# Kernel tuning notes

Hardware: AMD Instinct MI355X
Metric: run time of the kernel (lower is better)

Reference implementation:

```python
import jax, jax.numpy as jnp
import numpy as np

B, S, D, H = 2, 2048, 512, 8
HD = D // H
EPS = 1e-5


def _ln(x, g, b):
    mu = jnp.mean(x, axis=-1, keepdims=True)
    var = jnp.mean((x - mu) ** 2, axis=-1, keepdims=True)
    return (x - mu) * jax.lax.rsqrt(var + EPS) * g + b


def setup_inputs() -> dict:
    key = jax.random.key(0)
    ks = jax.random.split(key, 16)
    x = jax.random.normal(ks[0], (B, S, D), dtype=jnp.float32)
    adj = jax.random.randint(ks[1], (B, S, S), 0, 2, dtype=jnp.int32)
    adj = adj.at[:, jnp.arange(S), jnp.arange(S)].set(1)  # self-loops, avoid all-masked rows
    edge_attr = jax.random.normal(ks[2], (B, S, S), dtype=jnp.float32)
    sc = 1.0 / np.sqrt(D)
    p = lambda k, shp: jax.random.normal(k, shp, dtype=jnp.float32) * sc
    return {
        "x": x, "adj_matrix": adj, "edge_attr_matrix": edge_attr,
        "ln1_g": jnp.ones((D,)), "ln1_b": jnp.zeros((D,)),
        "ln2_g": jnp.ones((D,)), "ln2_b": jnp.zeros((D,)),
        "wq": p(ks[3], (D, D)), "bq": jnp.zeros((D,)),
        "wk": p(ks[4], (D, D)), "bk": jnp.zeros((D,)),
        "wv": p(ks[5], (D, D)), "bv": jnp.zeros((D,)),
        "wo": p(ks[6], (D, D)), "bo": jnp.zeros((D,)),
        "w1": p(ks[7], (D, 4 * D)), "b1": jnp.zeros((4 * D,)),
        "w2": p(ks[8], (4 * D, D)), "b2": jnp.zeros((D,)),
    }


def reference(x, adj_matrix, edge_attr_matrix, ln1_g, ln1_b, ln2_g, ln2_b,
              wq, bq, wk, bk, wv, bv, wo, bo, w1, b1, w2, b2):
    b, s, d = x.shape
    residual = x
    nx = _ln(x, ln1_g, ln1_b)
    q = (nx @ wq + bq).reshape(b, s, H, HD).transpose(0, 2, 1, 3)  # [B,H,S,HD]
    k = (nx @ wk + bk).reshape(b, s, H, HD).transpose(0, 2, 1, 3)
    v = (nx @ wv + bv).reshape(b, s, H, HD).transpose(0, 2, 1, 3)
    adjf = adj_matrix.astype(jnp.float32)
    # bias: -inf where no edge, else 0.1*edge_attr*adj (faithful to score_mod)
    bias = jnp.where(adj_matrix > 0, 0.1 * edge_attr_matrix * adjf, -jnp.inf)[:, None]  # [B,1,S,S]
    scores = jnp.einsum('bhqd,bhkd->bhqk', q, k) / np.sqrt(HD) + bias
    attn = jax.nn.softmax(scores, axis=-1)
    out = jnp.einsum('bhqk,bhkd->bhqd', attn, v)
    out = out.transpose(0, 2, 1, 3).reshape(b, s, d)
    x1 = residual + (out @ wo + bo)
    n2 = _ln(x1, ln2_g, ln2_b)
    mlp = jax.nn.gelu(n2 @ w1 + b1, approximate=False) @ w2 + b2
    return x1 + mlp
```

## Files before the change

kernel.cpp:

```cpp
#include <hip/hip_runtime.h>
#include <cstdint>
#include <cstddef>

typedef __bf16 bf16x8 __attribute__((ext_vector_type(8)));
typedef float f32x4 __attribute__((ext_vector_type(4)));
typedef const __attribute__((address_space(1))) void* gas_t;
typedef __attribute__((address_space(3))) void* las_t;

#define LOG2E 1.4426950408889634f
#define QSCALE 0.18033688011112042f
#define BSCALE 0.14426950408889634f

__device__ __forceinline__ unsigned short f2bf(float f) {
  union { float f; unsigned u; } v; v.f = f;
  unsigned r = v.u + 0x7FFFu + ((v.u >> 16) & 1u);
  return (unsigned short)(r >> 16);
}
__device__ __forceinline__ unsigned short f2bf_fast(float f) {
  union { float f; unsigned u; } v; v.f = f;
  return (unsigned short)((v.u + 0x8000u) >> 16);
}
__device__ __forceinline__ float bf2f(unsigned short h) {
  union { unsigned u; float f; } v; v.u = ((unsigned)h) << 16;
  return v.f;
}
__device__ __forceinline__ void gll16(const void* g, void* l) {
  __builtin_amdgcn_global_load_lds((gas_t)g, (las_t)l, 16, 0, 0);
}

__global__ __launch_bounds__(256) void transpose_cast(const float* __restrict__ in,
                                                      unsigned short* __restrict__ out,
                                                      int R, int C) {
  __shared__ float tile[32][33];
  int bx = blockIdx.x * 32, by = blockIdx.y * 32;
  int tx = threadIdx.x & 31, tg = threadIdx.x >> 5;
  #pragma unroll
  for (int i = 0; i < 4; i++) {
    int r = tg * 4 + i;
    tile[r][tx] = in[(size_t)(by + r) * C + bx + tx];
  }
  __syncthreads();
  #pragma unroll
  for (int i = 0; i < 4; i++) {
    int r = tg * 4 + i;
    out[(size_t)(bx + r) * R + by + tx] = f2bf(tile[tx][r]);
  }
}

struct TP4 { const float* in[4]; unsigned short* out[4]; };
__global__ __launch_bounds__(256) void transpose_cast4(TP4 p) {
  __shared__ float tile[32][33];
  const float* in = p.in[blockIdx.z];
  unsigned short* out = p.out[blockIdx.z];
  int bx = blockIdx.x * 32, by = blockIdx.y * 32;
  int tx = threadIdx.x & 31, tg = threadIdx.x >> 5;
  #pragma unroll
  for (int i = 0; i < 4; i++) {
    int r = tg * 4 + i;
    tile[r][tx] = in[(size_t)(by + r) * 512 + bx + tx];
  }
  __syncthreads();
  #pragma unroll
  for (int i = 0; i < 4; i++) {
    int r = tg * 4 + i;
    out[(size_t)(bx + r) * 512 + by + tx] = f2bf(tile[tx][r]);
  }
}

__global__ __launch_bounds__(256) void bias_pack(const int* __restrict__ adj,
                                                 const float* __restrict__ edge,
                                                 unsigned short* __restrict__ bp) {
  size_t i = ((size_t)blockIdx.x * 256 + threadIdx.x) * 4;
  int4 a = *(const int4*)(adj + i);
  float4 e = *(const float4*)(edge + i);
  ushort4 r;
  r.x = a.x > 0 ? f2bf(BSCALE * e.x * (float)a.x - 20.0f) : f2bf(-30000.0f);
  r.y = a.y > 0 ? f2bf(BSCALE * e.y * (float)a.y - 20.0f) : f2bf(-30000.0f);
  r.z = a.z > 0 ? f2bf(BSCALE * e.z * (float)a.z - 20.0f) : f2bf(-30000.0f);
  r.w = a.w > 0 ? f2bf(BSCALE * e.w * (float)a.w - 20.0f) : f2bf(-30000.0f);
  *(ushort4*)(bp + i) = r;
}

__global__ __launch_bounds__(256) void ln_kernel(const float* __restrict__ x,
                                                 const float* __restrict__ g,
                                                 const float* __restrict__ bt,
                                                 unsigned short* __restrict__ out,
                                                 const float* __restrict__ badd,
                                                 float* __restrict__ oinit) {
  int row = blockIdx.x, tid = threadIdx.x;
  const float* xr = x + (size_t)row * 512;
  float2 v = *(const float2*)(xr + tid * 2);
  float s = v.x + v.y, s2 = v.x * v.x + v.y * v.y;
  #pragma unroll
  for (int m = 1; m < 64; m <<= 1) { s += __shfl_xor(s, m, 64); s2 += __shfl_xor(s2, m, 64); }
  __shared__ float red[8];
  int w = tid >> 6;
  if ((tid & 63) == 0) { red[w * 2] = s; red[w * 2 + 1] = s2; }
  __syncthreads();
  float ts = red[0] + red[2] + red[4] + red[6];
  float ts2 = red[1] + red[3] + red[5] + red[7];
  float mu = ts * (1.0f / 512.0f);
  float rs = rsqrtf(ts2 * (1.0f / 512.0f) - mu * mu + 1e-5f);
  int c = tid * 2;
  ushort2 o;
  o.x = f2bf((v.x - mu) * rs * g[c] + bt[c]);
  o.y = f2bf((v.y - mu) * rs * g[c + 1] + bt[c + 1]);
  *(ushort2*)(out + (size_t)row * 512 + c) = o;
  if (oinit) {
    float2 oi; oi.x = v.x + badd[c]; oi.y = v.y + badd[c + 1];
    *(float2*)(oinit + (size_t)row * 512 + c) = oi;
  }
}

struct EpiQKV {
  unsigned short *q, *k, *v;
  const float *bq, *bk, *bv;
  __device__ void operator()(int m, int n, float val) const {
    int b = m >> 11, s = m & 2047;
    int which = n >> 9, col = n & 511;
    int h = col >> 6, d = col & 63;
    int bh = b * 8 + h;
    if (which == 0)      q[((size_t)bh * 2048 + s) * 64 + d] = f2bf((val + bq[col]) * QSCALE);
    else if (which == 1) k[((size_t)bh * 2048 + s) * 64 + d] = f2bf(val + bk[col]);
    else                 v[((size_t)bh * 2048 + s) * 64 + d] = f2bf(val + bv[col]);
  }
};
struct EpiAtomic {
  float* dst; int ldn;
  __device__ void operator()(int m, int n, float val) const {
    atomicAdd(dst + (size_t)m * ldn + n, val);
  }
};
struct EpiGelu {
  const float* b1; unsigned short* h;
  __device__ void operator()(int m, int n, float val) const {
    float t = val + b1[n];
    float gl = 0.5f * t * (1.0f + erff(t * 0.70710678118654752f));
    h[(size_t)m * 2048 + n] = f2bf(gl);
  }
};

template <typename Epi>
__global__ __launch_bounds__(256) void gemm_bt(const unsigned short* __restrict__ A,
                                               const unsigned short* __restrict__ Bt,
                                               int lda, int ldb, int kchunk, Epi epi) {
  __shared__ unsigned short a_lds[128 * 32];
  __shared__ unsigned short b_lds[128 * 32];
  const int tid = threadIdx.x;
  const int lane = tid & 63;
  const int w = tid >> 6;
  const int l15 = lane & 15, quad = lane >> 4;
  const int wm = w >> 1, wn = w & 1;
  const int m0 = blockIdx.y * 128, n0 = blockIdx.x * 128;
  const int K0 = blockIdx.z * kchunk, K1 = K0 + kchunk;

  f32x4 acc[4][4] = {};

  for (int k0 = K0; k0 < K1; k0 += 32) {
    __syncthreads();
    #pragma unroll
    for (int i = 0; i < 2; i++) {
      int c = tid + i * 256;
      int g = c >> 6;
      int row = g * 16 + l15;
      int col = quad * 8;
      gll16(A + (size_t)(m0 + row) * lda + k0 + col, a_lds + (size_t)(c & ~63) * 8);
      gll16(Bt + (size_t)(n0 + row) * ldb + k0 + col, b_lds + (size_t)(c & ~63) * 8);
    }
    __syncthreads();
    bf16x8 af[4], bfr[4];
    #pragma unroll
    for (int t = 0; t < 4; t++) {
      af[t]  = *(const bf16x8*)(a_lds + ((size_t)(wm * 4 + t) * 64 + lane) * 8);
      bfr[t] = *(const bf16x8*)(b_lds + ((size_t)(wn * 4 + t) * 64 + lane) * 8);
    }
    #pragma unroll
    for (int mt = 0; mt < 4; mt++)
      #pragma unroll
      for (int nt = 0; nt < 4; nt++)
        acc[mt][nt] = __builtin_amdgcn_mfma_f32_16x16x32_bf16(af[mt], bfr[nt], acc[mt][nt], 0, 0, 0);
  }
  #pragma unroll
  for (int mt = 0; mt < 4; mt++)
    #pragma unroll
    for (int nt = 0; nt < 4; nt++)
      #pragma unroll
      for (int r = 0; r < 4; r++)
        epi(m0 + wm * 64 + mt * 16 + quad * 4 + r, n0 + wn * 64 + nt * 16 + l15, acc[mt][nt][r]);
}

__global__ __launch_bounds__(256) void vt_kernel(const unsigned short* __restrict__ vb,
                                                 unsigned short* __restrict__ vbT) {
  __shared__ unsigned short tile[64][72];
  const int bh = blockIdx.y, s0 = blockIdx.x * 64;
  const int tid = threadIdx.x;
  const unsigned short* src = vb + ((size_t)bh * 2048 + s0) * 64;
  #pragma unroll
  for (int i = 0; i < 2; i++) {
    int r = (tid >> 3) + i * 32;
    int c8 = (tid & 7) * 8;
    *(uint4*)(&tile[r][c8]) = *(const uint4*)(src + (size_t)r * 64 + c8);
  }
  __syncthreads();
  unsigned short* dst = vbT + (size_t)bh * 64 * 2048 + s0;
  #pragma unroll
  for (int i = 0; i < 2; i++) {
    int d = (tid >> 3) + i * 32;
    int s8 = (tid & 7) * 8;
    ushort4 o0, o1;
    o0.x = tile[s8 + 0][d]; o0.y = tile[s8 + 1][d]; o0.z = tile[s8 + 2][d]; o0.w = tile[s8 + 3][d];
    o1.x = tile[s8 + 4][d]; o1.y = tile[s8 + 5][d]; o1.z = tile[s8 + 6][d]; o1.w = tile[s8 + 7][d];
    *(ushort4*)(dst + (size_t)d * 2048 + s8) = o0;
    *(ushort4*)(dst + (size_t)d * 2048 + s8 + 4) = o1;
  }
}

__global__ __launch_bounds__(256) void attn_kernel(const unsigned short* __restrict__ Q,
                                                   const unsigned short* __restrict__ Kb,
                                                   const unsigned short* __restrict__ VT,
                                                   const unsigned short* __restrict__ biasp,
                                                   float* __restrict__ o_part,
                                                   float* __restrict__ l_part) {
  __shared__ unsigned short k_lds[64 * 64];
  __shared__ unsigned short v_lds[64 * 64];
  __shared__ unsigned short bias_lds[128 * 72];
  __shared__ unsigned short p_lds[4][2][16 * 72];

  const int tid = threadIdx.x;
  const int lane = tid & 63, w = tid >> 6;
  const int l15 = lane & 15, quad = lane >> 4;
  const int bh = blockIdx.x, b = bh >> 3;
  const int q0 = blockIdx.y * 128;
  const int split = blockIdx.z;

  bf16x8 qf[2][2];
  #pragma unroll
  for (int g = 0; g < 2; g++) {
    const unsigned short* qrow = Q + ((size_t)bh * 2048 + q0 + w * 32 + g * 16 + l15) * 64;
    qf[g][0] = *(const bf16x8*)(qrow + quad * 8);
    qf[g][1] = *(const bf16x8*)(qrow + 32 + quad * 8);
  }

  f32x4 o_acc[2][4] = {};
  float l_acc[2] = {0.0f, 0.0f};

  const unsigned short* kbase = Kb + (size_t)bh * 2048 * 64;
  const unsigned short* vbase = VT + (size_t)bh * 64 * 2048;
  const unsigned short* bbase = biasp + ((size_t)b * 2048 + q0) * 2048;

  const int kt0 = split * 16, kt1 = kt0 + 16;
  for (int kt = kt0; kt < kt1; kt++) {
    const int kcol0 = kt * 64;
    __syncthreads();
    #pragma unroll
    for (int i = 0; i < 2; i++) {
      int c = tid + i * 256;
      int g = c >> 6;
      int mt = g >> 1, kk = g & 1;
      int rr = mt * 16 + l15;
      int cc = kk * 32 + quad * 8;
      gll16(kbase + (size_t)(kcol0 + rr) * 64 + cc, k_lds + (size_t)(c & ~63) * 8);
      gll16(vbase + (size_t)rr * 2048 + kcol0 + cc, v_lds + (size_t)(c & ~63) * 8);
    }
    #pragma unroll
    for (int i = 0; i < 4; i++) {
      int r = (tid >> 3) + i * 32;
      int c8 = (tid & 7) * 8;
      uint4 dv = *(const uint4*)(bbase + (size_t)r * 2048 + kcol0 + c8);
      *(uint4*)(bias_lds + r * 72 + c8) = dv;
    }
    __syncthreads();

    bf16x8 af[4][2];
    #pragma unroll
    for (int mt = 0; mt < 4; mt++) {
      af[mt][0] = *(const bf16x8*)(k_lds + ((size_t)(mt * 2 + 0) * 64 + lane) * 8);
      af[mt][1] = *(const bf16x8*)(k_lds + ((size_t)(mt * 2 + 1) * 64 + lane) * 8);
    }

    #pragma unroll
    for (int g = 0; g < 2; g++) {
      const int qrow = w * 32 + g * 16 + l15;
      #pragma unroll
      for (int mt = 0; mt < 4; mt++) {
        ushort4 bl = *(const ushort4*)(bias_lds + (size_t)qrow * 72 + mt * 16 + quad * 4);
        f32x4 cb; cb[0] = bf2f(bl.x); cb[1] = bf2f(bl.y); cb[2] = bf2f(bl.z); cb[3] = bf2f(bl.w);
        f32x4 accv = __builtin_amdgcn_mfma_f32_16x16x32_bf16(af[mt][0], qf[g][0], cb, 0, 0, 0);
        accv = __builtin_amdgcn_mfma_f32_16x16x32_bf16(af[mt][1], qf[g][1], accv, 0, 0, 0);
        float p0 = exp2f(accv[0]), p1 = exp2f(accv[1]);
        float p2 = exp2f(accv[2]), p3 = exp2f(accv[3]);
        l_acc[g] += (p0 + p1) + (p2 + p3);
        ushort4 pv;
        pv.x = f2bf_fast(p0); pv.y = f2bf_fast(p1); pv.z = f2bf_fast(p2); pv.w = f2bf_fast(p3);
        *(ushort4*)(p_lds[w][g] + l15 * 72 + mt * 16 + quad * 4) = pv;
      }
    }

    bf16x8 vf[4][2];
    #pragma unroll
    for (int dt = 0; dt < 4; dt++) {
      vf[dt][0] = *(const bf16x8*)(v_lds + ((size_t)(dt * 2 + 0) * 64 + lane) * 8);
      vf[dt][1] = *(const bf16x8*)(v_lds + ((size_t)(dt * 2 + 1) * 64 + lane) * 8);
    }
    #pragma unroll
    for (int g = 0; g < 2; g++) {
      bf16x8 pf0 = *(const bf16x8*)(p_lds[w][g] + l15 * 72 + quad * 8);
      bf16x8 pf1 = *(const bf16x8*)(p_lds[w][g] + l15 * 72 + 32 + quad * 8);
      #pragma unroll
      for (int dt = 0; dt < 4; dt++) {
        o_acc[g][dt] = __builtin_amdgcn_mfma_f32_16x16x32_bf16(pf0, vf[dt][0], o_acc[g][dt], 0, 0, 0);
        o_acc[g][dt] = __builtin_amdgcn_mfma_f32_16x16x32_bf16(pf1, vf[dt][1], o_acc[g][dt], 0, 0, 0);
      }
    }
  }

  const size_t obase = ((size_t)split * 16 + bh) * 2048;
  #pragma unroll
  for (int g = 0; g < 2; g++) {
    float l = l_acc[g];
    l += __shfl_xor(l, 16, 64);
    l += __shfl_xor(l, 32, 64);
    if (quad == 0) l_part[obase + q0 + w * 32 + g * 16 + l15] = l;
    #pragma unroll
    for (int dt = 0; dt < 4; dt++)
      #pragma unroll
      for (int r = 0; r < 4; r++)
        o_part[(obase + q0 + w * 32 + g * 16 + quad * 4 + r) * 64 + dt * 16 + l15] = o_acc[g][dt][r];
  }
}

__global__ __launch_bounds__(256) void combine_kernel(const float* __restrict__ o_part,
                                                      const float* __restrict__ l_part,
                                                      const float* __restrict__ x,
                                                      const float* __restrict__ bo,
                                                      unsigned short* __restrict__ ao,
                                                      float* __restrict__ x1) {
  const int row = blockIdx.x;
  const int b = row >> 11, s = row & 2047;
  const int col = threadIdx.x * 2;
  const int h = col >> 6, d = col & 63;
  const int bh = b * 8 + h;
  const size_t i0 = ((size_t)bh * 2048 + s) * 64 + d;
  const size_t i1 = ((size_t)(16 + bh) * 2048 + s) * 64 + d;
  float2 a = *(const float2*)(o_part + i0);
  float2 c = *(const float2*)(o_part + i1);
  float l = l_part[(size_t)bh * 2048 + s] + l_part[(size_t)(16 + bh) * 2048 + s];
  float inv = 1.0f / l;
  ushort2 o;
  o.x = f2bf((a.x + c.x) * inv);
  o.y = f2bf((a.y + c.y) * inv);
  *(ushort2*)(ao + (size_t)row * 512 + col) = o;
  float2 xv = *(const float2*)(x + (size_t)row * 512 + col);
  float2 xo; xo.x = xv.x + bo[col]; xo.y = xv.y + bo[col + 1];
  *(float2*)(x1 + (size_t)row * 512 + col) = xo;
}

extern "C" void kernel_launch(void* const* d_in, const int* in_sizes, int n_in,
                              void* d_out, int out_size, void* d_ws, size_t ws_size,
                              hipStream_t stream) {
  (void)in_sizes; (void)n_in; (void)out_size; (void)ws_size;
  const float* x    = (const float*)d_in[0];
  const int*   adj  = (const int*)d_in[1];
  const float* edge = (const float*)d_in[2];
  const float* ln1g = (const float*)d_in[3];
  const float* ln1b = (const float*)d_in[4];
  const float* ln2g = (const float*)d_in[5];
  const float* ln2b = (const float*)d_in[6];
  const float* wq = (const float*)d_in[7];  const float* bq = (const float*)d_in[8];
  const float* wk = (const float*)d_in[9];  const float* bk = (const float*)d_in[10];
  const float* wv = (const float*)d_in[11]; const float* bv = (const float*)d_in[12];
  const float* wo = (const float*)d_in[13]; const float* bo = (const float*)d_in[14];
  const float* w1 = (const float*)d_in[15]; const float* b1 = (const float*)d_in[16];
  const float* w2 = (const float*)d_in[17]; const float* b2 = (const float*)d_in[18];
  float* out = (float*)d_out;

  char* ws = (char*)d_ws;
  unsigned short* qkvT = (unsigned short*)ws; ws += (size_t)1536 * 512 * 2;
  unsigned short* woT  = (unsigned short*)ws; ws += (size_t)512 * 512 * 2;
  unsigned short* w1T  = (unsigned short*)ws; ws += (size_t)2048 * 512 * 2;
  unsigned short* w2T  = (unsigned short*)ws; ws += (size_t)512 * 2048 * 2;
  unsigned short* bp   = (unsigned short*)ws; ws += (size_t)2 * 2048 * 2048 * 2;
  unsigned short* nx   = (unsigned short*)ws; ws += (size_t)4096 * 512 * 2;
  unsigned short* qb   = (unsigned short*)ws; ws += (size_t)16 * 2048 * 64 * 2;
  unsigned short* kb   = (unsigned short*)ws; ws += (size_t)16 * 2048 * 64 * 2;
  unsigned short* vb   = (unsigned short*)ws; ws += (size_t)16 * 2048 * 64 * 2;
  unsigned short* vbT  = (unsigned short*)ws; ws += (size_t)16 * 64 * 2048 * 2;
  unsigned short* ao   = (unsigned short*)ws; ws += (size_t)4096 * 512 * 2;
  float*          x1   = (float*)ws;          ws += (size_t)4096 * 512 * 4;
  unsigned short* n2   = (unsigned short*)ws; ws += (size_t)4096 * 512 * 2;
  float*          lpt  = (float*)ws;          ws += (size_t)2 * 16 * 2048 * 4;
  float*          opt  = (float*)ws;
  unsigned short* hb   = (unsigned short*)opt;

  dim3 blk(256);
  TP4 tp; tp.in[0] = wq; tp.in[1] = wk; tp.in[2] = wv; tp.in[3] = wo;
  tp.out[0] = qkvT; tp.out[1] = qkvT + (size_t)512 * 512;
  tp.out[2] = qkvT + (size_t)2 * 512 * 512; tp.out[3] = woT;
  transpose_cast4<<<dim3(16, 16, 4), blk, 0, stream>>>(tp);
  transpose_cast<<<dim3(64, 16), blk, 0, stream>>>(w1, w1T, 512, 2048);
  transpose_cast<<<dim3(16, 64), blk, 0, stream>>>(w2, w2T, 2048, 512);
  bias_pack<<<8192, blk, 0, stream>>>(adj, edge, bp);
  ln_kernel<<<4096, blk, 0, stream>>>(x, ln1g, ln1b, nx, nullptr, nullptr);
  gemm_bt<<<dim3(12, 32, 1), blk, 0, stream>>>(nx, qkvT, 512, 512, 512,
                                               EpiQKV{qb, kb, vb, bq, bk, bv});
  vt_kernel<<<dim3(32, 16), blk, 0, stream>>>(vb, vbT);
  attn_kernel<<<dim3(16, 16, 2), blk, 0, stream>>>(qb, kb, vbT, bp, opt, lpt);
  combine_kernel<<<4096, blk, 0, stream>>>(opt, lpt, x, bo, ao, x1);
  gemm_bt<<<dim3(4, 32, 2), blk, 0, stream>>>(ao, woT, 512, 512, 256,
                                              EpiAtomic{x1, 512});
  ln_kernel<<<4096, blk, 0, stream>>>(x1, ln2g, ln2b, n2, b2, out);
  gemm_bt<<<dim3(16, 32, 1), blk, 0, stream>>>(n2, w1T, 512, 512, 512,
                                               EpiGelu{b1, hb});
  gemm_bt<<<dim3(4, 32, 4), blk, 0, stream>>>(hb, w2T, 2048, 2048, 512,
                                              EpiAtomic{out, 512});
}
```

Baseline: 357.0 us.

## Replace atomic split-K with bf16 partials, widen GEMM K-step, rework attention splits

Split-K GEMMs now write bf16 partial sums to separate buffers instead of doing fp32 atomicAdd. The partials are reduced in a fused residual+LayerNorm kernel and in a final combine kernel. The GEMM K-tile grows from 32 to 64 to halve the barrier count. Attention now uses 4 key splits with bf16 partial outputs, loads bias straight into registers instead of staging it in LDS, and adds an occupancy hint. The workspace is reorganised with aliasing, which risks overlap bugs and loses some precision from the bf16 partials.

```diff
diff --git a/kernel.cpp b/kernel.cpp
--- a/kernel.cpp
+++ b/kernel.cpp
@@ -7,7 +7,6 @@
 typedef const __attribute__((address_space(1))) void* gas_t;
 typedef __attribute__((address_space(3))) void* las_t;
 
-#define LOG2E 1.4426950408889634f
 #define QSCALE 0.18033688011112042f
 #define BSCALE 0.14426950408889634f
 
@@ -84,12 +83,9 @@
 __global__ __launch_bounds__(256) void ln_kernel(const float* __restrict__ x,
                                                  const float* __restrict__ g,
                                                  const float* __restrict__ bt,
-                                                 unsigned short* __restrict__ out,
-                                                 const float* __restrict__ badd,
-                                                 float* __restrict__ oinit) {
+                                                 unsigned short* __restrict__ out) {
   int row = blockIdx.x, tid = threadIdx.x;
-  const float* xr = x + (size_t)row * 512;
-  float2 v = *(const float2*)(xr + tid * 2);
+  float2 v = *(const float2*)(x + (size_t)row * 512 + tid * 2);
   float s = v.x + v.y, s2 = v.x * v.x + v.y * v.y;
   #pragma unroll
   for (int m = 1; m < 64; m <<= 1) { s += __shfl_xor(s, m, 64); s2 += __shfl_xor(s2, m, 64); }
@@ -106,10 +102,59 @@
   o.x = f2bf((v.x - mu) * rs * g[c] + bt[c]);
   o.y = f2bf((v.y - mu) * rs * g[c + 1] + bt[c + 1]);
   *(ushort2*)(out + (size_t)row * 512 + c) = o;
-  if (oinit) {
-    float2 oi; oi.x = v.x + badd[c]; oi.y = v.y + badd[c + 1];
-    *(float2*)(oinit + (size_t)row * 512 + c) = oi;
-  }
+}
+
+__global__ __launch_bounds__(256) void ln_fuse2(const float* __restrict__ x,
+                                                const unsigned short* __restrict__ opp,
+                                                const float* __restrict__ bo,
+                                                const float* __restrict__ g,
+                                                const float* __restrict__ bt,
+                                                float* __restrict__ x1,
+                                                unsigned short* __restrict__ n2) {
+  const size_t MN = (size_t)4096 * 512;
+  int row = blockIdx.x, tid = threadIdx.x;
+  int c = tid * 2;
+  size_t idx = (size_t)row * 512 + c;
+  float2 xv = *(const float2*)(x + idx);
+  ushort2 p0 = *(const ushort2*)(opp + idx);
+  ushort2 p1 = *(const ushort2*)(opp + MN + idx);
+  float2 v;
+  v.x = xv.x + bo[c]     + bf2f(p0.x) + bf2f(p1.x);
+  v.y = xv.y + bo[c + 1] + bf2f(p0.y) + bf2f(p1.y);
+  float s = v.x + v.y, s2 = v.x * v.x + v.y * v.y;
+  #pragma unroll
+  for (int m = 1; m < 64; m <<= 1) { s += __shfl_xor(s, m, 64); s2 += __shfl_xor(s2, m, 64); }
+  __shared__ float red[8];
+  int w = tid >> 6;
+  if ((tid & 63) == 0) { red[w * 2] = s; red[w * 2 + 1] = s2; }
+  __syncthreads();
+  float ts = red[0] + red[2] + red[4] + red[6];
+  float ts2 = red[1] + red[3] + red[5] + red[7];
+  float mu = ts * (1.0f / 512.0f);
+  float rs = rsqrtf(ts2 * (1.0f / 512.0f) - mu * mu + 1e-5f);
+  *(float2*)(x1 + idx) = v;
+  ushort2 o;
+  o.x = f2bf((v.x - mu) * rs * g[c] + bt[c]);
+  o.y = f2bf((v.y - mu) * rs * g[c + 1] + bt[c + 1]);
+  *(ushort2*)(n2 + idx) = o;
+}
+
+__global__ __launch_bounds__(256) void final_combine(const float* __restrict__ x1,
+                                                     const float* __restrict__ b2,
+                                                     const unsigned short* __restrict__ mp,
+                                                     float* __restrict__ out) {
+  const size_t MN = (size_t)4096 * 512;
+  size_t i = ((size_t)blockIdx.x * 256 + threadIdx.x) * 4;
+  float4 xv = *(const float4*)(x1 + i);
+  float4 bv = *(const float4*)(b2 + (i & 511));
+  float4 a;
+  a.x = xv.x + bv.x; a.y = xv.y + bv.y; a.z = xv.z + bv.z; a.w = xv.w + bv.w;
+  #pragma unroll
+  for (int sp = 0; sp < 4; sp++) {
+    ushort4 p = *(const ushort4*)(mp + sp * MN + i);
+    a.x += bf2f(p.x); a.y += bf2f(p.y); a.z += bf2f(p.z); a.w += bf2f(p.w);
+  }
+  *(float4*)(out + i) = a;
 }
 
 struct EpiQKV {
@@ -125,10 +170,10 @@
     else                 v[((size_t)bh * 2048 + s) * 64 + d] = f2bf(val + bv[col]);
   }
 };
-struct EpiAtomic {
-  float* dst; int ldn;
+struct EpiPart {
+  unsigned short* dst; int ldn;
   __device__ void operator()(int m, int n, float val) const {
-    atomicAdd(dst + (size_t)m * ldn + n, val);
+    dst[(size_t)blockIdx.z * 4096 * 512 + (size_t)m * ldn + n] = f2bf(val);
   }
 };
 struct EpiGelu {
@@ -144,8 +189,8 @@
 __global__ __launch_bounds__(256) void gemm_bt(const unsigned short* __restrict__ A,
                                                const unsigned short* __restrict__ Bt,
                                                int lda, int ldb, int kchunk, Epi epi) {
-  __shared__ unsigned short a_lds[128 * 32];
-  __shared__ unsigned short b_lds[128 * 32];
+  __shared__ unsigned short a_lds[128 * 64];
+  __shared__ unsigned short b_lds[128 * 64];
   const int tid = threadIdx.x;
   const int lane = tid & 63;
   const int w = tid >> 6;
@@ -156,29 +201,33 @@
 
   f32x4 acc[4][4] = {};
 
-  for (int k0 = K0; k0 < K1; k0 += 32) {
+  for (int k0 = K0; k0 < K1; k0 += 64) {
     __syncthreads();
     #pragma unroll
-    for (int i = 0; i < 2; i++) {
+    for (int i = 0; i < 4; i++) {
       int c = tid + i * 256;
       int g = c >> 6;
-      int row = g * 16 + l15;
-      int col = quad * 8;
+      int row = (g >> 1) * 16 + l15;
+      int col = (g & 1) * 32 + quad * 8;
       gll16(A + (size_t)(m0 + row) * lda + k0 + col, a_lds + (size_t)(c & ~63) * 8);
       gll16(Bt + (size_t)(n0 + row) * ldb + k0 + col, b_lds + (size_t)(c & ~63) * 8);
     }
     __syncthreads();
-    bf16x8 af[4], bfr[4];
-    #pragma unroll
-    for (int t = 0; t < 4; t++) {
-      af[t]  = *(const bf16x8*)(a_lds + ((size_t)(wm * 4 + t) * 64 + lane) * 8);
-      bfr[t] = *(const bf16x8*)(b_lds + ((size_t)(wn * 4 + t) * 64 + lane) * 8);
-    }
+    bf16x8 af[4][2], bfr[4][2];
+    #pragma unroll
+    for (int t = 0; t < 4; t++)
+      #pragma unroll
+      for (int ks = 0; ks < 2; ks++) {
+        af[t][ks]  = *(const bf16x8*)(a_lds + (((size_t)(wm * 4 + t) * 2 + ks) * 64 + lane) * 8);
+        bfr[t][ks] = *(const bf16x8*)(b_lds + (((size_t)(wn * 4 + t) * 2 + ks) * 64 + lane) * 8);
+      }
     #pragma unroll
     for (int mt = 0; mt < 4; mt++)
       #pragma unroll
-      for (int nt = 0; nt < 4; nt++)
-        acc[mt][nt] = __builtin_amdgcn_mfma_f32_16x16x32_bf16(af[mt], bfr[nt], acc[mt][nt], 0, 0, 0);
+      for (int nt = 0; nt < 4; nt++) {
+        acc[mt][nt] = __builtin_amdgcn_mfma_f32_16x16x32_bf16(af[mt][0], bfr[nt][0], acc[mt][nt], 0, 0, 0);
+        acc[mt][nt] = __builtin_amdgcn_mfma_f32_16x16x32_bf16(af[mt][1], bfr[nt][1], acc[mt][nt], 0, 0, 0);
+      }
   }
   #pragma unroll
   for (int mt = 0; mt < 4; mt++)
@@ -215,15 +264,14 @@
   }
 }
 
-__global__ __launch_bounds__(256) void attn_kernel(const unsigned short* __restrict__ Q,
-                                                   const unsigned short* __restrict__ Kb,
-                                                   const unsigned short* __restrict__ VT,
-                                                   const unsigned short* __restrict__ biasp,
-                                                   float* __restrict__ o_part,
-                                                   float* __restrict__ l_part) {
+__global__ __launch_bounds__(256, 4) void attn_kernel(const unsigned short* __restrict__ Q,
+                                                      const unsigned short* __restrict__ Kb,
+                                                      const unsigned short* __restrict__ VT,
+                                                      const unsigned short* __restrict__ biasp,
+                                                      unsigned short* __restrict__ o_part,
+                                                      float* __restrict__ l_part) {
   __shared__ unsigned short k_lds[64 * 64];
   __shared__ unsigned short v_lds[64 * 64];
-  __shared__ unsigned short bias_lds[128 * 72];
   __shared__ unsigned short p_lds[4][2][16 * 72];
 
   const int tid = threadIdx.x;
@@ -234,11 +282,13 @@
   const int split = blockIdx.z;
 
   bf16x8 qf[2][2];
+  const unsigned short* brow[2];
   #pragma unroll
   for (int g = 0; g < 2; g++) {
     const unsigned short* qrow = Q + ((size_t)bh * 2048 + q0 + w * 32 + g * 16 + l15) * 64;
     qf[g][0] = *(const bf16x8*)(qrow + quad * 8);
     qf[g][1] = *(const bf16x8*)(qrow + 32 + quad * 8);
+    brow[g] = biasp + ((size_t)b * 2048 + q0 + w * 32 + g * 16 + l15) * 2048;
   }
 
   f32x4 o_acc[2][4] = {};
@@ -246,9 +296,8 @@
 
   const unsigned short* kbase = Kb + (size_t)bh * 2048 * 64;
   const unsigned short* vbase = VT + (size_t)bh * 64 * 2048;
-  const unsigned short* bbase = biasp + ((size_t)b * 2048 + q0) * 2048;
-
-  const int kt0 = split * 16, kt1 = kt0 + 16;
+
+  const int kt0 = split * 8, kt1 = kt0 + 8;
   for (int kt = kt0; kt < kt1; kt++) {
     const int kcol0 = kt * 64;
     __syncthreads();
@@ -262,31 +311,25 @@
       gll16(kbase + (size_t)(kcol0 + rr) * 64 + cc, k_lds + (size_t)(c & ~63) * 8);
       gll16(vbase + (size_t)rr * 2048 + kcol0 + cc, v_lds + (size_t)(c & ~63) * 8);
     }
-    #pragma unroll
-    for (int i = 0; i < 4; i++) {
-      int r = (tid >> 3) + i * 32;
-      int c8 = (tid & 7) * 8;
-      uint4 dv = *(const uint4*)(bbase + (size_t)r * 2048 + kcol0 + c8);
-      *(uint4*)(bias_lds + r * 72 + c8) = dv;
-    }
+    ushort4 bl[2][4];
+    #pragma unroll
+    for (int g = 0; g < 2; g++)
+      #pragma unroll
+      for (int mt = 0; mt < 4; mt++)
+        bl[g][mt] = *(const ushort4*)(brow[g] + kcol0 + mt * 16 + quad * 4);
     __syncthreads();
 
-    bf16x8 af[4][2];
     #pragma unroll
     for (int mt = 0; mt < 4; mt++) {
-      af[mt][0] = *(const bf16x8*)(k_lds + ((size_t)(mt * 2 + 0) * 64 + lane) * 8);
-      af[mt][1] = *(const bf16x8*)(k_lds + ((size_t)(mt * 2 + 1) * 64 + lane) * 8);
-    }
-
-    #pragma unroll
-    for (int g = 0; g < 2; g++) {
-      const int qrow = w * 32 + g * 16 + l15;
-      #pragma unroll
-      for (int mt = 0; mt < 4; mt++) {
-        ushort4 bl = *(const ushort4*)(bias_lds + (size_t)qrow * 72 + mt * 16 + quad * 4);
-        f32x4 cb; cb[0] = bf2f(bl.x); cb[1] = bf2f(bl.y); cb[2] = bf2f(bl.z); cb[3] = bf2f(bl.w);
-        f32x4 accv = __builtin_amdgcn_mfma_f32_16x16x32_bf16(af[mt][0], qf[g][0], cb, 0, 0, 0);
-        accv = __builtin_amdgcn_mfma_f32_16x16x32_bf16(af[mt][1], qf[g][1], accv, 0, 0, 0);
+      bf16x8 a0 = *(const bf16x8*)(k_lds + ((size_t)(mt * 2 + 0) * 64 + lane) * 8);
+      bf16x8 a1 = *(const bf16x8*)(k_lds + ((size_t)(mt * 2 + 1) * 64 + lane) * 8);
+      #pragma unroll
+      for (int g = 0; g < 2; g++) {
+        f32x4 cb;
+        cb[0] = bf2f(bl[g][mt].x); cb[1] = bf2f(bl[g][mt].y);
+        cb[2] = bf2f(bl[g][mt].z); cb[3] = bf2f(bl[g][mt].w);
+        f32x4 accv = __builtin_amdgcn_mfma_f32_16x16x32_bf16(a0, qf[g][0], cb, 0, 0, 0);
+        accv = __builtin_amdgcn_mfma_f32_16x16x32_bf16(a1, qf[g][1], accv, 0, 0, 0);
         float p0 = exp2f(accv[0]), p1 = exp2f(accv[1]);
         float p2 = exp2f(accv[2]), p3 = exp2f(accv[3]);
         l_acc[g] += (p0 + p1) + (p2 + p3);
@@ -296,20 +339,20 @@
       }
     }
 
-    bf16x8 vf[4][2];
+    bf16x8 pf[2][2];
+    #pragma unroll
+    for (int g = 0; g < 2; g++) {
+      pf[g][0] = *(const bf16x8*)(p_lds[w][g] + l15 * 72 + quad * 8);
+      pf[g][1] = *(const bf16x8*)(p_lds[w][g] + l15 * 72 + 32 + quad * 8);
+    }
     #pragma unroll
     for (int dt = 0; dt < 4; dt++) {
-      vf[dt][0] = *(const bf16x8*)(v_lds + ((size_t)(dt * 2 + 0) * 64 + lane) * 8);
-      vf[dt][1] = *(const bf16x8*)(v_lds + ((size_t)(dt * 2 + 1) * 64 + lane) * 8);
-    }
-    #pragma unroll
-    for (int g = 0; g < 2; g++) {
-      bf16x8 pf0 = *(const bf16x8*)(p_lds[w][g] + l15 * 72 + quad * 8);
-      bf16x8 pf1 = *(const bf16x8*)(p_lds[w][g] + l15 * 72 + 32 + quad * 8);
-      #pragma unroll
-      for (int dt = 0; dt < 4; dt++) {
-        o_acc[g][dt] = __builtin_amdgcn_mfma_f32_16x16x32_bf16(pf0, vf[dt][0], o_acc[g][dt], 0, 0, 0);
-        o_acc[g][dt] = __builtin_amdgcn_mfma_f32_16x16x32_bf16(pf1, vf[dt][1], o_acc[g][dt], 0, 0, 0);
+      bf16x8 v0 = *(const bf16x8*)(v_lds + ((size_t)(dt * 2 + 0) * 64 + lane) * 8);
+      bf16x8 v1 = *(const bf16x8*)(v_lds + ((size_t)(dt * 2 + 1) * 64 + lane) * 8);
+      #pragma unroll
+      for (int g = 0; g < 2; g++) {
+        o_acc[g][dt] = __builtin_amdgcn_mfma_f32_16x16x32_bf16(pf[g][0], v0, o_acc[g][dt], 0, 0, 0);
+        o_acc[g][dt] = __builtin_amdgcn_mfma_f32_16x16x32_bf16(pf[g][1], v1, o_acc[g][dt], 0, 0, 0);
       }
     }
   }
@@ -325,34 +368,32 @@
     for (int dt = 0; dt < 4; dt++)
       #pragma unroll
       for (int r = 0; r < 4; r++)
-        o_part[(obase + q0 + w * 32 + g * 16 + quad * 4 + r) * 64 + dt * 16 + l15] = o_acc[g][dt][r];
-  }
-}
-
-__global__ __launch_bounds__(256) void combine_kernel(const float* __restrict__ o_part,
+        o_part[(obase + q0 + w * 32 + g * 16 + quad * 4 + r) * 64 + dt * 16 + l15] =
+            f2bf(o_acc[g][dt][r]);
+  }
+}
+
+__global__ __launch_bounds__(256) void combine_kernel(const unsigned short* __restrict__ o_part,
                                                       const float* __restrict__ l_part,
-                                                      const float* __restrict__ x,
-                                                      const float* __restrict__ bo,
-                                                      unsigned short* __restrict__ ao,
-                                                      float* __restrict__ x1) {
+                                                      unsigned short* __restrict__ ao) {
   const int row = blockIdx.x;
   const int b = row >> 11, s = row & 2047;
   const int col = threadIdx.x * 2;
   const int h = col >> 6, d = col & 63;
   const int bh = b * 8 + h;
-  const size_t i0 = ((size_t)bh * 2048 + s) * 64 + d;
-  const size_t i1 = ((size_t)(16 + bh) * 2048 + s) * 64 + d;
-  float2 a = *(const float2*)(o_part + i0);
-  float2 c = *(const float2*)(o_part + i1);
-  float l = l_part[(size_t)bh * 2048 + s] + l_part[(size_t)(16 + bh) * 2048 + s];
+  float ox = 0.0f, oy = 0.0f, l = 0.0f;
+  #pragma unroll
+  for (int sp = 0; sp < 4; sp++) {
+    size_t base = (size_t)(sp * 16 + bh) * 2048 + s;
+    ushort2 o = *(const ushort2*)(o_part + base * 64 + d);
+    ox += bf2f(o.x); oy += bf2f(o.y);
+    l += l_part[base];
+  }
   float inv = 1.0f / l;
   ushort2 o;
-  o.x = f2bf((a.x + c.x) * inv);
-  o.y = f2bf((a.y + c.y) * inv);
+  o.x = f2bf(ox * inv);
+  o.y = f2bf(oy * inv);
   *(ushort2*)(ao + (size_t)row * 512 + col) = o;
-  float2 xv = *(const float2*)(x + (size_t)row * 512 + col);
-  float2 xo; xo.x = xv.x + bo[col]; xo.y = xv.y + bo[col + 1];
-  *(float2*)(x1 + (size_t)row * 512 + col) = xo;
 }
 
 extern "C" void kernel_launch(void* const* d_in, const int* in_sizes, int n_in,
@@ -379,18 +420,21 @@
   unsigned short* woT  = (unsigned short*)ws; ws += (size_t)512 * 512 * 2;
   unsigned short* w1T  = (unsigned short*)ws; ws += (size_t)2048 * 512 * 2;
   unsigned short* w2T  = (unsigned short*)ws; ws += (size_t)512 * 2048 * 2;
-  unsigned short* bp   = (unsigned short*)ws; ws += (size_t)2 * 2048 * 2048 * 2;
-  unsigned short* nx   = (unsigned short*)ws; ws += (size_t)4096 * 512 * 2;
-  unsigned short* qb   = (unsigned short*)ws; ws += (size_t)16 * 2048 * 64 * 2;
-  unsigned short* kb   = (unsigned short*)ws; ws += (size_t)16 * 2048 * 64 * 2;
-  unsigned short* vb   = (unsigned short*)ws; ws += (size_t)16 * 2048 * 64 * 2;
-  unsigned short* vbT  = (unsigned short*)ws; ws += (size_t)16 * 64 * 2048 * 2;
+  unsigned short* bp   = (unsigned short*)ws;
+  unsigned short* opp  = (unsigned short*)ws; ws += (size_t)2 * 2048 * 2048 * 2;
+  unsigned short* nx   = (unsigned short*)ws;
+  unsigned short* n2   = (unsigned short*)ws; ws += (size_t)4096 * 512 * 2;
+  unsigned short* qb   = (unsigned short*)ws;
   unsigned short* ao   = (unsigned short*)ws; ws += (size_t)4096 * 512 * 2;
-  float*          x1   = (float*)ws;          ws += (size_t)4096 * 512 * 4;
-  unsigned short* n2   = (unsigned short*)ws; ws += (size_t)4096 * 512 * 2;
-  float*          lpt  = (float*)ws;          ws += (size_t)2 * 16 * 2048 * 4;
-  float*          opt  = (float*)ws;
-  unsigned short* hb   = (unsigned short*)opt;
+  unsigned short* kb   = (unsigned short*)ws; ws += (size_t)4096 * 512 * 2;
+  unsigned short* vb   = (unsigned short*)ws;
+  float*          x1   = (float*)ws;          ws += (size_t)4096 * 512 * 2;
+  unsigned short* vbT  = (unsigned short*)ws; ws += (size_t)4096 * 512 * 2;
+  char* region1 = ws;
+  unsigned short* opt  = (unsigned short*)region1;
+  unsigned short* hb   = (unsigned short*)region1;
+  float*          lpt  = (float*)(region1 + (size_t)4 * 16 * 2048 * 64 * 2);
+  unsigned short* mp   = (unsigned short*)(region1 + (size_t)4 * 16 * 2048 * 64 * 2);
 
   dim3 blk(256);
   TP4 tp; tp.in[0] = wq; tp.in[1] = wk; tp.in[2] = wv; tp.in[3] = wo;
@@ -400,17 +444,18 @@
   transpose_cast<<<dim3(64, 16), blk, 0, stream>>>(w1, w1T, 512, 2048);
   transpose_cast<<<dim3(16, 64), blk, 0, stream>>>(w2, w2T, 2048, 512);
   bias_pack<<<8192, blk, 0, stream>>>(adj, edge, bp);
-  ln_kernel<<<4096, blk, 0, stream>>>(x, ln1g, ln1b, nx, nullptr, nullptr);
+  ln_kernel<<<4096, blk, 0, stream>>>(x, ln1g, ln1b, nx);
   gemm_bt<<<dim3(12, 32, 1), blk, 0, stream>>>(nx, qkvT, 512, 512, 512,
                                                EpiQKV{qb, kb, vb, bq, bk, bv});
   vt_kernel<<<dim3(32, 16), blk, 0, stream>>>(vb, vbT);
-  attn_kernel<<<dim3(16, 16, 2), blk, 0, stream>>>(qb, kb, vbT, bp, opt, lpt);
-  combine_kernel<<<4096, blk, 0, stream>>>(opt, lpt, x, bo, ao, x1);
+  attn_kernel<<<dim3(16, 16, 4), blk, 0, stream>>>(qb, kb, vbT, bp, opt, lpt);
+  combine_kernel<<<4096, blk, 0, stream>>>(opt, lpt, ao);
   gemm_bt<<<dim3(4, 32, 2), blk, 0, stream>>>(ao, woT, 512, 512, 256,
-                                              EpiAtomic{x1, 512});
-  ln_kernel<<<4096, blk, 0, stream>>>(x1, ln2g, ln2b, n2, b2, out);
+                                              EpiPart{opp, 512});
+  ln_fuse2<<<4096, blk, 0, stream>>>(x, opp, bo, ln2g, ln2b, x1, n2);
   gemm_bt<<<dim3(16, 32, 1), blk, 0, stream>>>(n2, w1T, 512, 512, 512,
                                                EpiGelu{b1, hb});
   gemm_bt<<<dim3(4, 32, 4), blk, 0, stream>>>(hb, w2T, 2048, 2048, 512,
-                                              EpiAtomic{out, 512});
-}
+                                              EpiPart{mp, 512});
+  final_combine<<<2048, blk, 0, stream>>>(x1, b2, mp, out);
+}
```

Result: faster. 321.7 us (-9.9%).
